# Performance work log

Hardware: AMD Instinct MI355X
Metric: run time of the kernel (lower is better)

The kernel has to match this reference:

```python
import jax, jax.numpy as jnp
import numpy as np

B, T, C = 4, 2048, 1024
E, K, HID = 8, 2, 4096  # n_expert, top-k, mult*dim


def setup_inputs() -> dict:
    key = jax.random.key(0)
    ks = jax.random.split(key, 9)
    s = 1.0 / np.sqrt(C)
    sh = 1.0 / np.sqrt(HID)
    return {
        "x": jax.random.normal(ks[0], (B, T, C), jnp.float32),
        "wg_w": jax.random.normal(ks[1], (C, E), jnp.float32) * s,
        "wg_b": jnp.zeros((E,), jnp.float32),
        "w1": jax.random.normal(ks[2], (E, C, HID), jnp.float32) * s,
        "b1": jnp.zeros((E, HID), jnp.float32),
        "w3": jax.random.normal(ks[3], (E, C, HID), jnp.float32) * s,
        "b3": jnp.zeros((E, HID), jnp.float32),
        "w2": jax.random.normal(ks[4], (E, HID, C), jnp.float32) * sh,
        "b2": jnp.zeros((E, C), jnp.float32),
    }


def reference(x, wg_w, wg_b, w1, b1, w3, b3, w2, b2):
    Bx, Tx, Cx = x.shape
    xf = x.reshape(-1, Cx)                       # (S, C)
    S = xf.shape[0]
    # --- TopKGate ---
    logits = xf @ wg_w + wg_b                    # (S, E)
    probs = jax.nn.softmax(logits, axis=-1)
    vals, idx = jax.lax.top_k(probs, K)          # (S, K)
    importance = probs.mean(axis=0)              # (E,)
    load = jnp.zeros((E,), probs.dtype).at[idx[:, 0]].add(1.0) / S
    aux = E * (importance * load).sum()
    # per-token per-expert combine weight (top-k ids are unique per row)
    w_full = jnp.zeros((S, E), probs.dtype).at[jnp.arange(S)[:, None], idx].add(vals)
    # --- experts: SwiGLU FFN, loop over small fixed E ---
    y = jnp.zeros_like(xf)
    for e in range(E):
        h = jax.nn.silu(xf @ w1[e] + b1[e]) * (xf @ w3[e] + b3[e])  # (S, HID)
        y = y + w_full[:, e:e + 1] * (h @ w2[e] + b2[e])
    return y.reshape(Bx, Tx, Cx), aux
```

## Files before the change

kernel.cpp:

```cpp
#include <hip/hip_runtime.h>

#define S_TOK 8192
#define C_DIM 1024
#define E_NUM 8
#define HID_DIM 4096

typedef unsigned short u16;
typedef __bf16 bf16x8 __attribute__((ext_vector_type(8)));
typedef float f32x4 __attribute__((ext_vector_type(4)));

__device__ __forceinline__ u16 f2bf(float f){
  union { float f; unsigned u; } v; v.f = f;
  unsigned r = v.u + 0x7fffu + ((v.u >> 16) & 1u);
  return (u16)(r >> 16);
}
__device__ __forceinline__ float bf2f(u16 b){
  union { unsigned u; float f; } v; v.u = ((unsigned)b) << 16; return v.f;
}

__device__ __forceinline__ void async_copy16(const void* g, void* l){
  __builtin_amdgcn_global_load_lds((const __attribute__((address_space(1))) void*)g,
                                   (__attribute__((address_space(3))) void*)l, 16, 0, 0);
}

__global__ __launch_bounds__(256) void gate_kernel(
    const float* __restrict__ x, const float* __restrict__ wg_w, const float* __restrict__ wg_b,
    u16* __restrict__ xb,
    int* __restrict__ top_idx, float* __restrict__ top_val,
    float* __restrict__ imp_sum, int* __restrict__ cnt_top1, int* __restrict__ counts)
{
  __shared__ float s_imp[E_NUM];
  __shared__ int   s_c1[E_NUM], s_cnt[E_NUM];
  if (threadIdx.x < E_NUM){ s_imp[threadIdx.x]=0.f; s_c1[threadIdx.x]=0; s_cnt[threadIdx.x]=0; }
  __syncthreads();

  int wid = threadIdx.x >> 6, lane = threadIdx.x & 63;
  int t = blockIdx.x * 4 + wid;
  const float4* xr4 = (const float4*)(x + (size_t)t * C_DIM);
  u16* xbr = xb + (size_t)t * C_DIM;
  float acc[E_NUM];
  #pragma unroll
  for (int e=0;e<E_NUM;e++) acc[e]=0.f;
  #pragma unroll
  for (int c4 = 0; c4 < C_DIM/4/64; c4++){
    int c = (c4*64 + lane);
    float4 xv = xr4[c];
    ushort4 o = make_ushort4(f2bf(xv.x), f2bf(xv.y), f2bf(xv.z), f2bf(xv.w));
    *(ushort4*)&xbr[c*4] = o;
    const float* wr = wg_w + (size_t)c * 4 * E_NUM;
    #pragma unroll
    for (int e=0;e<E_NUM;e++)
      acc[e] += xv.x*wr[e] + xv.y*wr[E_NUM+e] + xv.z*wr[2*E_NUM+e] + xv.w*wr[3*E_NUM+e];
  }
  #pragma unroll
  for (int e=0;e<E_NUM;e++){
    float v = acc[e];
    #pragma unroll
    for (int off=32; off>0; off>>=1) v += __shfl_xor(v, off, 64);
    acc[e] = v + wg_b[e];
  }
  float mx = acc[0];
  #pragma unroll
  for (int e=1;e<E_NUM;e++) mx = fmaxf(mx, acc[e]);
  float sum = 0.f;
  #pragma unroll
  for (int e=0;e<E_NUM;e++){ acc[e] = __expf(acc[e]-mx); sum += acc[e]; }
  float inv = 1.f/sum;
  #pragma unroll
  for (int e=0;e<E_NUM;e++) acc[e] *= inv;
  int i1=0; float v1=acc[0];
  #pragma unroll
  for (int e=1;e<E_NUM;e++) if (acc[e] > v1){ v1=acc[e]; i1=e; }
  int i2=-1; float v2=-1.f;
  #pragma unroll
  for (int e=0;e<E_NUM;e++) if (e!=i1 && acc[e] > v2){ v2=acc[e]; i2=e; }

  if (lane==0){
    top_idx[t*2+0]=i1; top_idx[t*2+1]=i2;
    top_val[t*2+0]=v1; top_val[t*2+1]=v2;
    #pragma unroll
    for (int e=0;e<E_NUM;e++) atomicAdd(&s_imp[e], acc[e]);
    atomicAdd(&s_c1[i1],1);
    atomicAdd(&s_cnt[i1],1); atomicAdd(&s_cnt[i2],1);
  }
  __syncthreads();
  if (threadIdx.x < E_NUM){
    atomicAdd(&imp_sum[threadIdx.x], s_imp[threadIdx.x]);
    atomicAdd(&cnt_top1[threadIdx.x], s_c1[threadIdx.x]);
    atomicAdd(&counts[threadIdx.x], s_cnt[threadIdx.x]);
  }
}

__global__ void scan_kernel(const int* __restrict__ counts, int* __restrict__ offsets,
                            int* __restrict__ cursor, const float* __restrict__ imp_sum,
                            const int* __restrict__ cnt_top1, float* __restrict__ aux_out)
{
  if (threadIdx.x==0 && blockIdx.x==0){
    int off=0;
    #pragma unroll
    for (int e=0;e<E_NUM;e++){ offsets[e]=off; cursor[e]=off; off+=counts[e]; }
    float aux=0.f;
    #pragma unroll
    for (int e=0;e<E_NUM;e++)
      aux += (imp_sum[e]/(float)S_TOK) * ((float)cnt_top1[e]/(float)S_TOK);
    aux_out[0] = aux * (float)E_NUM;
  }
}

__global__ __launch_bounds__(256) void scatter_kernel(
    const int* __restrict__ top_idx, const float* __restrict__ top_val,
    int* __restrict__ cursor, int* __restrict__ token_list, float* __restrict__ token_w,
    int* __restrict__ pos_of_slot)
{
  int t = blockIdx.x*256 + threadIdx.x;
  #pragma unroll
  for (int k=0;k<2;k++){
    int e = top_idx[t*2+k];
    int pos = atomicAdd(&cursor[e], 1);
    token_list[pos] = t;
    token_w[pos]    = top_val[t*2+k];
    pos_of_slot[t*2+k] = pos;
  }
}

__global__ __launch_bounds__(256) void transpose_kernel(const float* __restrict__ in, u16* __restrict__ out,
                                                        int R, int Cc)
{
  __shared__ float tile[64][65];
  int e = blockIdx.z;
  const float* src = in  + (size_t)e*R*Cc;
  u16*         dst = out + (size_t)e*R*Cc;
  int c0 = blockIdx.x*64, r0 = blockIdx.y*64;
  int tx = threadIdx.x, ty = threadIdx.y;
  #pragma unroll
  for (int i = ty; i < 64; i += 16){
    float4 v = *(const float4*)&src[(size_t)(r0+i)*Cc + c0 + tx*4];
    tile[i][tx*4+0] = v.x; tile[i][tx*4+1] = v.y;
    tile[i][tx*4+2] = v.z; tile[i][tx*4+3] = v.w;
  }
  __syncthreads();
  #pragma unroll
  for (int i = ty; i < 64; i += 16){
    ushort4 o = make_ushort4(f2bf(tile[tx*4+0][i]), f2bf(tile[tx*4+1][i]),
                             f2bf(tile[tx*4+2][i]), f2bf(tile[tx*4+3][i]));
    *(ushort4*)&dst[(size_t)(c0+i)*R + r0 + tx*4] = o;
  }
}


__global__ __launch_bounds__(512,1) void gemm1_kernel(
    const u16* __restrict__ xb, const u16* __restrict__ w1t, const u16* __restrict__ w3t,
    const float* __restrict__ b1, const float* __restrict__ b3,
    const int* __restrict__ token_list, const int* __restrict__ offsets, const int* __restrict__ counts,
    u16* __restrict__ h)
{
  int e  = blockIdx.z;
  int Ne = counts[e];
  int m0 = blockIdx.y * 128;
  if (m0 >= Ne) return;
  int seg = offsets[e];
  int n0  = blockIdx.x * 128;

  __shared__ u16 lA [128*64];
  __shared__ u16 lB1[128*64];
  __shared__ u16 lB3[128*64];

  int tid = threadIdx.x;
  int wid = tid >> 6, lane = tid & 63;
  int wr = wid >> 2, wc = wid & 3;

  const int srcsw = (((lane&7) ^ ((lane>>3)&7))) * 8;

  size_t gA[2], gB[2];
  #pragma unroll
  for (int i=0;i<2;i++){
    int r  = wid*16 + i*8 + (lane>>3);
    int rr = m0 + r; if (rr > Ne-1) rr = Ne-1;
    int tok = token_list[seg + rr];
    gA[i] = (size_t)tok * C_DIM + srcsw;
    int n  = n0 + wid*16 + i*8 + (lane>>3);
    gB[i] = ((size_t)e*HID_DIM + n) * C_DIM + srcsw;
  }

  f32x4 acc1[4][2], acc3[4][2];
  #pragma unroll
  for (int a=0;a<4;a++)
    #pragma unroll
    for (int b=0;b<2;b++){ acc1[a][b] = (f32x4){0.f,0.f,0.f,0.f}; acc3[a][b] = (f32x4){0.f,0.f,0.f,0.f}; }

  for (int k0=0; k0<C_DIM; k0+=64){
    #pragma unroll
    for (int i=0;i<2;i++){
      int lds_off = (wid*16 + i*8) * 64;
      async_copy16(xb  + gA[i] + k0, &lA [lds_off]);
      async_copy16(w1t + gB[i] + k0, &lB1[lds_off]);
      async_copy16(w3t + gB[i] + k0, &lB3[lds_off]);
    }
    __syncthreads();
    #pragma unroll
    for (int ks=0; ks<2; ks++){
      int kkS = ((ks*4 + (lane>>4)) ^ (lane&7)) * 8;
      bf16x8 af[4], b1f[2], b3f[2];
      #pragma unroll
      for (int mi=0;mi<4;mi++) af[mi]  = *(const bf16x8*)&lA [(wr*64+mi*16+(lane&15))*64 + kkS];
      #pragma unroll
      for (int nj=0;nj<2;nj++){ b1f[nj] = *(const bf16x8*)&lB1[(wc*32+nj*16+(lane&15))*64 + kkS];
                                b3f[nj] = *(const bf16x8*)&lB3[(wc*32+nj*16+(lane&15))*64 + kkS]; }
      #pragma unroll
      for (int mi=0;mi<4;mi++)
        #pragma unroll
        for (int nj=0;nj<2;nj++){
          acc1[mi][nj] = __builtin_amdgcn_mfma_f32_16x16x32_bf16(af[mi], b1f[nj], acc1[mi][nj], 0,0,0);
          acc3[mi][nj] = __builtin_amdgcn_mfma_f32_16x16x32_bf16(af[mi], b3f[nj], acc3[mi][nj], 0,0,0);
        }
    }
    __syncthreads();
  }

  const float* b1p = b1 + (size_t)e*HID_DIM + n0;
  const float* b3p = b3 + (size_t)e*HID_DIM + n0;
  #pragma unroll
  for (int nj=0;nj<2;nj++){
    int nl = wc*32 + nj*16 + (lane&15);
    float bb1 = b1p[nl], bb3 = b3p[nl];
    #pragma unroll
    for (int mi=0;mi<4;mi++){
      #pragma unroll
      for (int r=0;r<4;r++){
        int ml = wr*64 + mi*16 + (lane>>4)*4 + r;
        int m  = m0 + ml;
        if (m < Ne){
          float a = acc1[mi][nj][r] + bb1;
          float b = acc3[mi][nj][r] + bb3;
          float hv = (a / (1.f + __expf(-a))) * b;
          h[(size_t)(seg+m)*HID_DIM + n0 + nl] = f2bf(hv);
        }
      }
    }
  }
}

__global__ __launch_bounds__(512,1) void gemm2_kernel(
    const u16* __restrict__ h, const u16* __restrict__ w2t, const float* __restrict__ b2,
    const float* __restrict__ token_w,
    const int* __restrict__ offsets, const int* __restrict__ counts,
    u16* __restrict__ ybuf)
{
  int e  = blockIdx.z;
  int Ne = counts[e];
  int m0 = blockIdx.y * 128;
  if (m0 >= Ne) return;
  int seg = offsets[e];
  int n0  = blockIdx.x * 128;

  __shared__ u16 lA[128*64];
  __shared__ u16 lB[128*64];
  int tid=threadIdx.x, wid=tid>>6, lane=tid&63, wr=wid>>2, wc=wid&3;

  const int srcsw = (((lane&7) ^ ((lane>>3)&7))) * 8;

  size_t gA[2], gB[2];
  #pragma unroll
  for (int i=0;i<2;i++){
    int r  = wid*16 + i*8 + (lane>>3);
    int rr = m0 + r; if (rr > Ne-1) rr = Ne-1;
    gA[i] = (size_t)(seg + rr)*HID_DIM + srcsw;
    int n  = n0 + wid*16 + i*8 + (lane>>3);
    gB[i] = ((size_t)e*C_DIM + n) * HID_DIM + srcsw;
  }

  f32x4 acc[4][2];
  #pragma unroll
  for (int a=0;a<4;a++)
    #pragma unroll
    for (int b=0;b<2;b++) acc[a][b] = (f32x4){0.f,0.f,0.f,0.f};

  for (int k0=0; k0<HID_DIM; k0+=64){
    #pragma unroll
    for (int i=0;i<2;i++){
      int lds_off = (wid*16 + i*8) * 64;
      async_copy16(h   + gA[i] + k0, &lA[lds_off]);
      async_copy16(w2t + gB[i] + k0, &lB[lds_off]);
    }
    __syncthreads();
    #pragma unroll
    for (int ks=0; ks<2; ks++){
      int kkS = ((ks*4 + (lane>>4)) ^ (lane&7)) * 8;
      bf16x8 af[4], bf[2];
      #pragma unroll
      for (int mi=0;mi<4;mi++) af[mi] = *(const bf16x8*)&lA[(wr*64+mi*16+(lane&15))*64 + kkS];
      #pragma unroll
      for (int nj=0;nj<2;nj++) bf[nj] = *(const bf16x8*)&lB[(wc*32+nj*16+(lane&15))*64 + kkS];
      #pragma unroll
      for (int mi=0;mi<4;mi++)
        #pragma unroll
        for (int nj=0;nj<2;nj++)
          acc[mi][nj] = __builtin_amdgcn_mfma_f32_16x16x32_bf16(af[mi], bf[nj], acc[mi][nj], 0,0,0);
    }
    __syncthreads();
  }

  const float* b2p = b2 + (size_t)e*C_DIM + n0;
  #pragma unroll
  for (int mi=0;mi<4;mi++){
    #pragma unroll
    for (int r=0;r<4;r++){
      int ml = wr*64 + mi*16 + (lane>>4)*4 + r;
      int m  = m0 + ml;
      if (m < Ne){
        float w = token_w[seg+m];
        #pragma unroll
        for (int nj=0;nj<2;nj++){
          int nl = wc*32 + nj*16 + (lane&15);
          ybuf[(size_t)(seg+m)*C_DIM + n0 + nl] = f2bf((acc[mi][nj][r] + b2p[nl]) * w);
        }
      }
    }
  }
}

__global__ __launch_bounds__(256) void combine_kernel(
    const u16* __restrict__ ybuf, const int* __restrict__ pos_of_slot, float* __restrict__ y)
{
  int t = blockIdx.x;
  int p0 = pos_of_slot[t*2+0], p1 = pos_of_slot[t*2+1];
  int c = threadIdx.x;
  ushort4 a = ((const ushort4*)(ybuf + (size_t)p0*C_DIM))[c];
  ushort4 b = ((const ushort4*)(ybuf + (size_t)p1*C_DIM))[c];
  float4 o = make_float4(bf2f(a.x)+bf2f(b.x), bf2f(a.y)+bf2f(b.y),
                         bf2f(a.z)+bf2f(b.z), bf2f(a.w)+bf2f(b.w));
  ((float4*)(y + (size_t)t*C_DIM))[c] = o;
}

extern "C" void kernel_launch(void* const* d_in, const int* in_sizes, int n_in,
                              void* d_out, int out_size, void* d_ws, size_t ws_size,
                              hipStream_t stream)
{
  const float* x    = (const float*)d_in[0];
  const float* wg_w = (const float*)d_in[1];
  const float* wg_b = (const float*)d_in[2];
  const float* w1   = (const float*)d_in[3];
  const float* b1   = (const float*)d_in[4];
  const float* w3   = (const float*)d_in[5];
  const float* b3   = (const float*)d_in[6];
  const float* w2   = (const float*)d_in[7];
  const float* b2   = (const float*)d_in[8];

  float* y   = (float*)d_out;
  float* aux = y + (size_t)S_TOK*C_DIM;

  char* ws = (char*)d_ws;
  size_t off = 0;
  auto alloc = [&](size_t bytes) -> void* {
    void* p = ws + off;
    off += (bytes + 255) & ~(size_t)255;
    return p;
  };
  u16*  xb        = (u16*)  alloc((size_t)S_TOK*C_DIM*2);
  u16*  w1t       = (u16*)  alloc((size_t)E_NUM*HID_DIM*C_DIM*2);
  u16*  w3t       = (u16*)  alloc((size_t)E_NUM*HID_DIM*C_DIM*2);
  u16*  w2t       = (u16*)  alloc((size_t)E_NUM*C_DIM*HID_DIM*2);
  u16*  h         = (u16*)  alloc((size_t)S_TOK*2*HID_DIM*2);
  int*  token_list= (int*)  alloc((size_t)S_TOK*2*4);
  float* token_w  = (float*)alloc((size_t)S_TOK*2*4);
  int*  top_idx   = (int*)  alloc((size_t)S_TOK*2*4);
  float* top_val  = (float*)alloc((size_t)S_TOK*2*4);
  int*  pos_of_slot=(int*)  alloc((size_t)S_TOK*2*4);
  char* stats     = (char*) alloc(4096);
  float* imp_sum  = (float*)(stats);
  int*   cnt1     = (int*)  (stats + 64);
  int*   counts   = (int*)  (stats + 128);
  int*   offsets  = (int*)  (stats + 192);
  int*   cursor   = (int*)  (stats + 256);
  u16* ybuf = (u16*)w1t;
  (void)in_sizes; (void)n_in; (void)out_size; (void)ws_size;

  hipMemsetAsync(stats, 0, 512, stream);

  dim3 tb(16,16);
  transpose_kernel<<<dim3(HID_DIM/64, C_DIM/64, E_NUM), tb, 0, stream>>>(w1, w1t, C_DIM, HID_DIM);
  transpose_kernel<<<dim3(HID_DIM/64, C_DIM/64, E_NUM), tb, 0, stream>>>(w3, w3t, C_DIM, HID_DIM);
  transpose_kernel<<<dim3(C_DIM/64, HID_DIM/64, E_NUM), tb, 0, stream>>>(w2, w2t, HID_DIM, C_DIM);

  gate_kernel<<<S_TOK/4, 256, 0, stream>>>(x, wg_w, wg_b, xb, top_idx, top_val, imp_sum, cnt1, counts);
  scan_kernel<<<1, 64, 0, stream>>>(counts, offsets, cursor, imp_sum, cnt1, aux);
  scatter_kernel<<<S_TOK/256, 256, 0, stream>>>(top_idx, top_val, cursor, token_list, token_w, pos_of_slot);

  gemm1_kernel<<<dim3(HID_DIM/128, S_TOK/128, E_NUM), 512, 0, stream>>>(
      xb, w1t, w3t, b1, b3, token_list, offsets, counts, h);
  gemm2_kernel<<<dim3(C_DIM/128, S_TOK/128, E_NUM), 512, 0, stream>>>(
      h, w2t, b2, token_w, offsets, counts, ybuf);
  combine_kernel<<<S_TOK, 256, 0, stream>>>(ybuf, pos_of_slot, y);
}
```

Before: 815.4 us.

## Multi-buffer LDS tiles with async prefetch pipelines in both expert GEMMs

Converts the single-buffered load-sync-compute loops in gemm1 and gemm2 into 3-stage and 4-stage software pipelines. Several K tiles are prefetched into LDS ring buffers with global_load_lds, and explicit vmcnt waits plus raw barriers replace __syncthreads, so memory latency overlaps with MFMA work. It also raises wave priority around the MFMA blocks. LDS use grows to 144 KB for gemm1 and 128 KB for gemm2, and correctness now depends on the hand-counted vmcnt values matching the number of outstanding loads.

```diff
diff --git a/kernel.cpp b/kernel.cpp
--- a/kernel.cpp
+++ b/kernel.cpp
@@ -22,6 +22,11 @@
   __builtin_amdgcn_global_load_lds((const __attribute__((address_space(1))) void*)g,
                                    (__attribute__((address_space(3))) void*)l, 16, 0, 0);
 }
+
+#define WAIT_VM(N) asm volatile("s_waitcnt vmcnt(" #N ")" ::: "memory")
+#define BAR_ENTER() do{ asm volatile("" ::: "memory"); __builtin_amdgcn_s_barrier(); \
+                        __builtin_amdgcn_sched_barrier(0); }while(0)
+#define BAR_EXIT()  do{ asm volatile("" ::: "memory"); __builtin_amdgcn_s_barrier(); }while(0)
 
 __global__ __launch_bounds__(256) void gate_kernel(
     const float* __restrict__ x, const float* __restrict__ wg_w, const float* __restrict__ wg_b,
@@ -161,9 +166,9 @@
   int seg = offsets[e];
   int n0  = blockIdx.x * 128;
 
-  __shared__ u16 lA [128*64];
-  __shared__ u16 lB1[128*64];
-  __shared__ u16 lB3[128*64];
+  __shared__ u16 lA [3][128*64];
+  __shared__ u16 lB1[3][128*64];
+  __shared__ u16 lB3[3][128*64];
 
   int tid = threadIdx.x;
   int wid = tid >> 6, lane = tid & 63;
@@ -188,24 +193,28 @@
     #pragma unroll
     for (int b=0;b<2;b++){ acc1[a][b] = (f32x4){0.f,0.f,0.f,0.f}; acc3[a][b] = (f32x4){0.f,0.f,0.f,0.f}; }
 
-  for (int k0=0; k0<C_DIM; k0+=64){
+  auto STAGE = [&](int t, int b){
+    int k0 = t*64;
     #pragma unroll
     for (int i=0;i<2;i++){
       int lds_off = (wid*16 + i*8) * 64;
-      async_copy16(xb  + gA[i] + k0, &lA [lds_off]);
-      async_copy16(w1t + gB[i] + k0, &lB1[lds_off]);
-      async_copy16(w3t + gB[i] + k0, &lB3[lds_off]);
-    }
-    __syncthreads();
+      async_copy16(xb  + gA[i] + k0, &lA [b][lds_off]);
+      async_copy16(w1t + gB[i] + k0, &lB1[b][lds_off]);
+      async_copy16(w3t + gB[i] + k0, &lB3[b][lds_off]);
+    }
+  };
+
+  auto COMPUTE = [&](int b){
     #pragma unroll
     for (int ks=0; ks<2; ks++){
       int kkS = ((ks*4 + (lane>>4)) ^ (lane&7)) * 8;
       bf16x8 af[4], b1f[2], b3f[2];
       #pragma unroll
-      for (int mi=0;mi<4;mi++) af[mi]  = *(const bf16x8*)&lA [(wr*64+mi*16+(lane&15))*64 + kkS];
-      #pragma unroll
-      for (int nj=0;nj<2;nj++){ b1f[nj] = *(const bf16x8*)&lB1[(wc*32+nj*16+(lane&15))*64 + kkS];
-                                b3f[nj] = *(const bf16x8*)&lB3[(wc*32+nj*16+(lane&15))*64 + kkS]; }
+      for (int mi=0;mi<4;mi++) af[mi]  = *(const bf16x8*)&lA [b][(wr*64+mi*16+(lane&15))*64 + kkS];
+      #pragma unroll
+      for (int nj=0;nj<2;nj++){ b1f[nj] = *(const bf16x8*)&lB1[b][(wc*32+nj*16+(lane&15))*64 + kkS];
+                                b3f[nj] = *(const bf16x8*)&lB3[b][(wc*32+nj*16+(lane&15))*64 + kkS]; }
+      __builtin_amdgcn_s_setprio(1);
       #pragma unroll
       for (int mi=0;mi<4;mi++)
         #pragma unroll
@@ -213,9 +222,25 @@
           acc1[mi][nj] = __builtin_amdgcn_mfma_f32_16x16x32_bf16(af[mi], b1f[nj], acc1[mi][nj], 0,0,0);
           acc3[mi][nj] = __builtin_amdgcn_mfma_f32_16x16x32_bf16(af[mi], b3f[nj], acc3[mi][nj], 0,0,0);
         }
-    }
-    __syncthreads();
-  }
+      __builtin_amdgcn_s_setprio(0);
+    }
+  };
+
+  const int NT = C_DIM/64;
+  STAGE(0,0); STAGE(1,1);
+  int cb = 0, sb = 2;
+  #pragma unroll 1
+  for (int t=0; t<NT-2; ++t){
+    STAGE(t+2, sb);
+    WAIT_VM(12);
+    BAR_ENTER();
+    COMPUTE(cb);
+    BAR_EXIT();
+    cb = (cb+1==3)?0:cb+1; sb = (sb+1==3)?0:sb+1;
+  }
+  WAIT_VM(6);  BAR_ENTER(); COMPUTE(cb); BAR_EXIT();
+  cb = (cb+1==3)?0:cb+1;
+  WAIT_VM(0);  BAR_ENTER(); COMPUTE(cb);
 
   const float* b1p = b1 + (size_t)e*HID_DIM + n0;
   const float* b3p = b3 + (size_t)e*HID_DIM + n0;
@@ -253,8 +278,8 @@
   int seg = offsets[e];
   int n0  = blockIdx.x * 128;
 
-  __shared__ u16 lA[128*64];
-  __shared__ u16 lB[128*64];
+  __shared__ u16 lA[4][128*64];
+  __shared__ u16 lB[4][128*64];
   int tid=threadIdx.x, wid=tid>>6, lane=tid&63, wr=wid>>2, wc=wid&3;
 
   const int srcsw = (((lane&7) ^ ((lane>>3)&7))) * 8;
@@ -275,30 +300,48 @@
     #pragma unroll
     for (int b=0;b<2;b++) acc[a][b] = (f32x4){0.f,0.f,0.f,0.f};
 
-  for (int k0=0; k0<HID_DIM; k0+=64){
+  auto STAGE = [&](int t, int b){
+    int k0 = t*64;
     #pragma unroll
     for (int i=0;i<2;i++){
       int lds_off = (wid*16 + i*8) * 64;
-      async_copy16(h   + gA[i] + k0, &lA[lds_off]);
-      async_copy16(w2t + gB[i] + k0, &lB[lds_off]);
-    }
-    __syncthreads();
+      async_copy16(h   + gA[i] + k0, &lA[b][lds_off]);
+      async_copy16(w2t + gB[i] + k0, &lB[b][lds_off]);
+    }
+  };
+
+  auto COMPUTE = [&](int b){
     #pragma unroll
     for (int ks=0; ks<2; ks++){
       int kkS = ((ks*4 + (lane>>4)) ^ (lane&7)) * 8;
       bf16x8 af[4], bf[2];
       #pragma unroll
-      for (int mi=0;mi<4;mi++) af[mi] = *(const bf16x8*)&lA[(wr*64+mi*16+(lane&15))*64 + kkS];
-      #pragma unroll
-      for (int nj=0;nj<2;nj++) bf[nj] = *(const bf16x8*)&lB[(wc*32+nj*16+(lane&15))*64 + kkS];
+      for (int mi=0;mi<4;mi++) af[mi] = *(const bf16x8*)&lA[b][(wr*64+mi*16+(lane&15))*64 + kkS];
+      #pragma unroll
+      for (int nj=0;nj<2;nj++) bf[nj] = *(const bf16x8*)&lB[b][(wc*32+nj*16+(lane&15))*64 + kkS];
+      __builtin_amdgcn_s_setprio(1);
       #pragma unroll
       for (int mi=0;mi<4;mi++)
         #pragma unroll
         for (int nj=0;nj<2;nj++)
           acc[mi][nj] = __builtin_amdgcn_mfma_f32_16x16x32_bf16(af[mi], bf[nj], acc[mi][nj], 0,0,0);
-    }
-    __syncthreads();
-  }
+      __builtin_amdgcn_s_setprio(0);
+    }
+  };
+
+  const int NT = HID_DIM/64;
+  STAGE(0,0); STAGE(1,1); STAGE(2,2);
+  #pragma unroll 1
+  for (int t=0; t<NT-3; ++t){
+    STAGE(t+3, (t+3)&3);
+    WAIT_VM(12);
+    BAR_ENTER();
+    COMPUTE(t&3);
+    BAR_EXIT();
+  }
+  WAIT_VM(8);  BAR_ENTER(); COMPUTE((NT-3)&3); BAR_EXIT();
+  WAIT_VM(4);  BAR_ENTER(); COMPUTE((NT-2)&3); BAR_EXIT();
+  WAIT_VM(0);  BAR_ENTER(); COMPUTE((NT-1)&3);
 
   const float* b2p = b2 + (size_t)e*C_DIM + n0;
   #pragma unroll
```

Measured after the change: 1.116 ms. 36.8% more time.
